# Optimization experiments

Hardware: AMD Instinct MI355X
Metric: run time of the kernel (lower is better)

## Reference

```python
import jax, jax.numpy as jnp
import numpy as np

NUM_MOVIES = 100000
MOVIE_FEAT = 128
USER_FEAT = 128
BATCH = 16384
N_NBRS = 50
D0, D1, D2 = 256, 256, 128  # layer_dims


def setup_inputs() -> dict:
    key = jax.random.key(0)
    ks = jax.random.split(key, 16)
    inp = {
        "users": jax.random.normal(ks[0], (BATCH, USER_FEAT), jnp.float32),
        "pos_movies": jax.random.normal(ks[1], (BATCH, MOVIE_FEAT), jnp.float32),
        "neg_movies": jax.random.normal(ks[2], (BATCH, MOVIE_FEAT), jnp.float32),
        "user_ids": jax.random.randint(ks[3], (BATCH,), 0, BATCH),
        "pos_movie_ids": jax.random.randint(ks[4], (BATCH,), 0, NUM_MOVIES),
        "neg_movie_ids": jax.random.randint(ks[5], (BATCH,), 0, NUM_MOVIES),
        "nbr_ids": jax.random.randint(ks[6], (BATCH, N_NBRS), 0, NUM_MOVIES),
        # learned params / buffers
        "movie_table": jax.random.normal(ks[7], (NUM_MOVIES, MOVIE_FEAT), jnp.float32),
        "Wu": jax.random.normal(ks[8], (USER_FEAT, D0), jnp.float32) * (1.0 / np.sqrt(USER_FEAT)),
        "bu": jnp.zeros((D0,), jnp.float32),
        "Wm": jax.random.normal(ks[9], (MOVIE_FEAT, D0), jnp.float32) * (1.0 / np.sqrt(MOVIE_FEAT)),
        "bm": jnp.zeros((D0,), jnp.float32),
        "W1": jax.random.normal(ks[10], (D0, D1), jnp.float32) * (1.0 / np.sqrt(D0)),
        "b1": jnp.zeros((D1,), jnp.float32),
        "W2": jax.random.normal(ks[11], (D1, D2), jnp.float32) * (1.0 / np.sqrt(D1)),
        "b2": jnp.zeros((D2,), jnp.float32),
    }
    return inp


def reference(users, pos_movies, neg_movies, user_ids, pos_movie_ids, neg_movie_ids,
              nbr_ids, movie_table, Wu, bu, Wm, bm, W1, b1, W2, b2):
    # user_projection / movie_projection
    user_emb = users @ Wu + bu                      # [B, D0]
    movie_emb = movie_table @ Wm + bm               # [N, D0]
    pos_emb = movie_emb[pos_movie_ids]              # [B, D0]
    neg_emb = movie_emb[neg_movie_ids]              # [B, D0]
    # vectorized replacement of the per-user neighbor gather + mean loop
    nbr_mean = jnp.mean(movie_emb[nbr_ids], axis=1)  # [B, N_NBRS, D0] -> [B, D0]
    user_emb = user_emb + nbr_mean
    x = jnp.stack([user_emb, pos_emb, neg_emb], axis=0)  # [3, B, D0]
    x = jax.nn.relu(x @ W1 + b1)
    x = jax.nn.relu(x @ W2 + b2)
    return (x[0], x[1], x[2])
```

## Files before the change

### kernel.cpp

```cpp
#include <hip/hip_runtime.h>
#include <hip/hip_bf16.h>

#define BATCH_N   16384
#define FEAT      128
#define NNBR      50
#define NUM_MOVIES_N 100000

typedef short  short8  __attribute__((ext_vector_type(8)));
typedef float  floatx4 __attribute__((ext_vector_type(4)));
typedef unsigned int u32;

__device__ __forceinline__ __hip_bfloat16 f2bf(float x) { return __float2bfloat16(x); }
__device__ __forceinline__ float bfb2f(short s) {
  union { u32 u; float f; } c; c.u = ((u32)(unsigned short)s) << 16; return c.f;
}

__device__ __forceinline__ void gld16(const __hip_bfloat16* g, __hip_bfloat16* l) {
  __builtin_amdgcn_global_load_lds(
      (const __attribute__((address_space(1))) u32*)g,
      (__attribute__((address_space(3))) u32*)l, 16, 0, 0);
}

__device__ __forceinline__ floatx4 mfma16(short8 a, short8 b, floatx4 c) {
  return __builtin_amdgcn_mfma_f32_16x16x32_bf16(a, b, c, 0, 0, 0);
}

#define WAITVM2 asm volatile("s_waitcnt vmcnt(2)" ::: "memory")
#define WAITVM0 asm volatile("s_waitcnt vmcnt(0)" ::: "memory")

#define CONV_BLOCKS (NUM_MOVIES_N * FEAT / (256 * 8))
__global__ __launch_bounds__(256) void prep_all(
    const float* __restrict__ t, __hip_bfloat16* __restrict__ tb,
    const float* __restrict__ Wu, const float* __restrict__ Wm,
    const float* __restrict__ W1, const float* __restrict__ W2,
    const float* __restrict__ bu, const float* __restrict__ bm,
    __hip_bfloat16* __restrict__ WcatT, __hip_bfloat16* __restrict__ WmT,
    __hip_bfloat16* __restrict__ W1T,  __hip_bfloat16* __restrict__ W2T,
    float* __restrict__ bc) {
  int bid = blockIdx.x;
  if (bid < CONV_BLOCKS) {
    size_t i = ((size_t)bid * 256 + threadIdx.x) * 8;
    float4 v0 = *(const float4*)(t + i);
    float4 v1 = *(const float4*)(t + i + 4);
    __hip_bfloat16 o[8];
    o[0] = f2bf(v0.x); o[1] = f2bf(v0.y); o[2] = f2bf(v0.z); o[3] = f2bf(v0.w);
    o[4] = f2bf(v1.x); o[5] = f2bf(v1.y); o[6] = f2bf(v1.z); o[7] = f2bf(v1.w);
    *(short8*)(tb + i) = *(short8*)o;
  } else {
    int idx = (bid - CONV_BLOCKS) * 256 + threadIdx.x;
    int n = idx & 255, k = idx >> 8;
    float v = (k < 128) ? Wu[k * 256 + n] : Wm[(k - 128) * 256 + n];
    WcatT[n * 256 + k] = f2bf(v);
    W1T[n * 256 + k]   = f2bf(W1[k * 256 + n]);
    if (k < 128) WmT[n * 128 + k] = f2bf(Wm[k * 256 + n]);
    if (idx < 32768) {
      int k2 = idx >> 7, n2 = idx & 127;
      W2T[n2 * 256 + k2] = f2bf(W2[k2 * 128 + n2]);
    }
    if (idx < 256) bc[idx] = bu[idx] + bm[idx];
  }
}

template <int K0, int NCOL, bool RELU, bool TOGLB>
__device__ __forceinline__ void layer(
    const __hip_bfloat16* Ain,
    const __hip_bfloat16* __restrict__ Wt, const float* __restrict__ bias,
    __hip_bfloat16* Olds, float* __restrict__ Oglb,
    int wid, int quad, int lrow) {
  constexpr int KK = K0 / 32;
  constexpr int JN = NCOL / 128;
  const int c0 = wid * JN * 16;

  short8 bfr[JN][KK];
  float  bv[JN];
  #pragma unroll
  for (int j = 0; j < JN; ++j) {
    #pragma unroll
    for (int kc = 0; kc < KK; ++kc)
      bfr[j][kc] = *(const short8*)(Wt + (size_t)(c0 + j * 16 + lrow) * K0 +
                                    kc * 32 + quad * 8);
    bv[j] = bias[c0 + j * 16 + lrow];
  }

  #pragma unroll
  for (int it = 0; it < 4; ++it) {
    int r = it * 16 + lrow;
    short8 af[KK];
    #pragma unroll
    for (int kc = 0; kc < KK; ++kc)
      af[kc] = *(const short8*)&Ain[r * K0 + (((kc * 4 + quad) ^ (r & 7)) << 3)];
    floatx4 pa[JN], pb[JN];
    #pragma unroll
    for (int j = 0; j < JN; ++j) { pa[j] = {}; pb[j] = {}; }
    #pragma unroll
    for (int kc = 0; kc < KK; kc += 2)
      #pragma unroll
      for (int j = 0; j < JN; ++j) {
        pa[j] = mfma16(af[kc],     bfr[j][kc],     pa[j]);
        pb[j] = mfma16(af[kc + 1], bfr[j][kc + 1], pb[j]);
      }
    #pragma unroll
    for (int j = 0; j < JN; ++j) {
      floatx4 a = pa[j] + pb[j];
      int col = c0 + j * 16 + lrow;
      #pragma unroll
      for (int rr = 0; rr < 4; ++rr) {
        int row = it * 16 + quad * 4 + rr;
        float v = a[rr] + bv[j];
        if (RELU) v = fmaxf(v, 0.f);
        if (TOGLB) {
          Oglb[(size_t)row * NCOL + col] = v;
        } else {
          int ch = col >> 3;
          Olds[row * 256 + (((ch ^ (row & 7)) << 3) | (col & 7))] = f2bf(v);
        }
      }
    }
  }
}

__global__ __launch_bounds__(512)
__attribute__((amdgpu_waves_per_eu(2, 2)))
void fused_mlp(
    const float* __restrict__ users,
    const __hip_bfloat16* __restrict__ tb,
    const int* __restrict__ pos_ids, const int* __restrict__ neg_ids,
    const int* __restrict__ nbr_ids,
    const __hip_bfloat16* __restrict__ WcatT,
    const __hip_bfloat16* __restrict__ WmT,
    const __hip_bfloat16* __restrict__ W1T,
    const __hip_bfloat16* __restrict__ W2T,
    const float* __restrict__ bc, const float* __restrict__ bmv,
    const float* __restrict__ b1, const float* __restrict__ b2,
    float* __restrict__ out) {
  __shared__ __hip_bfloat16 A_lds[64 * 256];
  __shared__ __hip_bfloat16 E_lds[64 * 256];

  const int t    = threadIdx.x;
  const int lane = t & 63, wid = t >> 6;
  const int quad = lane >> 4, lrow = lane & 15;

  int s, tile;
  if (blockIdx.x < 256) { s = 0; tile = blockIdx.x; }
  else { int k = blockIdx.x - 256; s = 1 + (k & 1); tile = k >> 1; }
  const long m0 = (long)tile * 64;

  if (s == 0) {
    const int rbase = wid << 3;
    const int* nbw = nbr_ids + (size_t)(m0 + rbase) * NNBR;
    int idreg[7];
    #pragma unroll
    for (int w = 0; w < 7; ++w) {
      int fl = w * 64 + lane;
      idreg[w] = nbw[fl < 8 * NNBR ? fl : 8 * NNBR - 1];
    }
    float2 uvr[8];
    #pragma unroll
    for (int r = 0; r < 8; ++r)
      uvr[r] = ((const float2*)(users + (size_t)(m0 + rbase + r) * FEAT))[lane];

    __hip_bfloat16* stg = E_lds + (wid << 11);

    auto getid = [&](int fb) -> int {
      int idx = fb + quad;
      int v = __shfl(idreg[fb >> 6], idx & 63, 64);
      if ((fb >> 6) != ((fb + 3) >> 6)) {
        int v2 = __shfl(idreg[(fb + 3) >> 6], idx & 63, 64);
        v = ((idx >> 6) == (fb >> 6)) ? v : v2;
      }
      return v;
    };
    auto issue = [&](int k) {
      int row = k / 7, c = k % 7;
      int id0 = getid(row * NNBR + c * 8);
      int id1 = getid(row * NNBR + c * 8 + 4);
      __hip_bfloat16* dst = stg + ((k & 1) << 10);
      gld16(tb + (size_t)id0 * FEAT + (lrow << 3), dst + (lane << 3));
      gld16(tb + (size_t)id1 * FEAT + (lrow << 3), dst + 512 + (lane << 3));
    };

    issue(0); issue(1);
    float acc[8] = {0.f, 0.f, 0.f, 0.f, 0.f, 0.f, 0.f, 0.f};
    #pragma unroll
    for (int k = 0; k < 56; ++k) {
      if (k < 55) { WAITVM2; } else { WAITVM0; }
      const __hip_bfloat16* b = stg + ((k & 1) << 10);
      int c = k % 7;
      short8 x0 = *(const short8*)(b + (lane << 3));
      if (c < 6) {
        short8 x1 = *(const short8*)(b + 512 + (lane << 3));
        #pragma unroll
        for (int e = 0; e < 8; ++e) { acc[e] += bfb2f(x0[e]); acc[e] += bfb2f(x1[e]); }
      } else if (quad < 2) {
        #pragma unroll
        for (int e = 0; e < 8; ++e) acc[e] += bfb2f(x0[e]);
      }
      if (c == 6) {
        int row = k / 7, r = rbase + row;
        __hip_bfloat16 o[8];
        #pragma unroll
        for (int e = 0; e < 8; ++e) {
          float v = acc[e];
          v += __shfl_xor(v, 16, 64);
          v += __shfl_xor(v, 32, 64);
          o[e] = f2bf(v * (1.f / NNBR));
          acc[e] = 0.f;
        }
        if (quad == 0) {
          int ch = 16 + lrow;
          *(short8*)(A_lds + r * 256 + ((ch ^ (r & 7)) << 3)) = *(short8*)o;
        }
        float2 uv = uvr[row];
        __hip_bfloat162 t0; t0.x = f2bf(uv.x); t0.y = f2bf(uv.y);
        int col = lane << 1, ch2 = col >> 3;
        *(__hip_bfloat162*)(A_lds + r * 256 + ((ch2 ^ (r & 7)) << 3) + (col & 7)) = t0;
      }
      __builtin_amdgcn_sched_barrier(0);
      if (k + 2 < 56) issue(k + 2);
    }
  } else {
    const int* ids = (s == 1) ? pos_ids : neg_ids;
    #pragma unroll
    for (int i = 0; i < 2; ++i) {
      int c = t + i * 512;
      int r = c >> 4, sl = c & 15;
      int id = ids[m0 + r];
      gld16(tb + ((size_t)id << 7) + ((sl ^ (r & 7)) << 3),
            A_lds + (c << 3));
    }
  }
  __syncthreads();

  if (s == 0)
    layer<256, 256, false, false>(A_lds, WcatT, bc, E_lds, nullptr,
                                  wid, quad, lrow);
  else
    layer<128, 256, false, false>(A_lds, WmT, bmv, E_lds, nullptr,
                                  wid, quad, lrow);
  __syncthreads();

  layer<256, 256, true, false>(E_lds, W1T, b1, A_lds, nullptr,
                               wid, quad, lrow);
  __syncthreads();

  layer<256, 128, true, true>(A_lds, W2T, b2, nullptr,
                              out + ((size_t)s * BATCH_N + m0) * 128,
                              wid, quad, lrow);
}

extern "C" void kernel_launch(void* const* d_in, const int* in_sizes, int n_in,
                              void* d_out, int out_size, void* d_ws, size_t ws_size,
                              hipStream_t stream) {
  const float* users   = (const float*)d_in[0];
  const int*   pos_ids = (const int*)d_in[4];
  const int*   neg_ids = (const int*)d_in[5];
  const int*   nbr_ids = (const int*)d_in[6];
  const float* table   = (const float*)d_in[7];
  const float* Wu = (const float*)d_in[8];
  const float* bu = (const float*)d_in[9];
  const float* Wm = (const float*)d_in[10];
  const float* bm = (const float*)d_in[11];
  const float* W1 = (const float*)d_in[12];
  const float* b1 = (const float*)d_in[13];
  const float* W2 = (const float*)d_in[14];
  const float* b2 = (const float*)d_in[15];
  float* out = (float*)d_out;

  char* p = (char*)d_ws;
  auto carve = [&](size_t bytes) { char* r = p; p += (bytes + 255) & ~(size_t)255; return r; };
  __hip_bfloat16* tb     = (__hip_bfloat16*)carve((size_t)NUM_MOVIES_N * FEAT * 2);
  __hip_bfloat16* WcatT  = (__hip_bfloat16*)carve(256 * 256 * 2);
  __hip_bfloat16* WmT    = (__hip_bfloat16*)carve(256 * 128 * 2);
  __hip_bfloat16* W1T    = (__hip_bfloat16*)carve(256 * 256 * 2);
  __hip_bfloat16* W2T    = (__hip_bfloat16*)carve(128 * 256 * 2);
  float*          bc     = (float*)carve(256 * 4);

  prep_all<<<CONV_BLOCKS + 256, 256, 0, stream>>>(
      table, tb, Wu, Wm, W1, W2, bu, bm, WcatT, WmT, W1T, W2T, bc);
  fused_mlp<<<3 * BATCH_N / 64, 512, 0, stream>>>(
      users, tb, pos_ids, neg_ids, nbr_ids, WcatT, WmT, W1T, W2T,
      bc, bm, b1, b2, out);
}
```

Measured before the change: 193.4 us.

## Halve user-tile rows and interleave user and movie blocks for load balance

User-path blocks, which do the expensive 50-neighbor gather, now handle 32 rows instead of 64, so their gather loop is half as long. User and pos/neg blocks are interleaved by block index so the heavy and light tiles are spread across the grid. The grid grows to 1024 blocks and the layer template gains a row-count parameter. The smaller user tiles load the weight fragments more times per row and use the MFMA units less efficiently in the MLP layers.

```diff
diff --git a/kernel.cpp b/kernel.cpp
--- a/kernel.cpp
+++ b/kernel.cpp
@@ -61,7 +61,7 @@
   }
 }
 
-template <int K0, int NCOL, bool RELU, bool TOGLB>
+template <int MROWS, int K0, int NCOL, bool RELU, bool TOGLB>
 __device__ __forceinline__ void layer(
     const __hip_bfloat16* Ain,
     const __hip_bfloat16* __restrict__ Wt, const float* __restrict__ bias,
@@ -83,7 +83,7 @@
   }
 
   #pragma unroll
-  for (int it = 0; it < 4; ++it) {
+  for (int it = 0; it < MROWS / 16; ++it) {
     int r = it * 16 + lrow;
     short8 af[KK];
     #pragma unroll
@@ -133,30 +133,31 @@
     const float* __restrict__ bc, const float* __restrict__ bmv,
     const float* __restrict__ b1, const float* __restrict__ b2,
     float* __restrict__ out) {
-  __shared__ __hip_bfloat16 A_lds[64 * 256];
-  __shared__ __hip_bfloat16 E_lds[64 * 256];
+  __shared__ char raw[65536];
+  __hip_bfloat16* A_lds = (__hip_bfloat16*)raw;
+  __hip_bfloat16* E_lds = (__hip_bfloat16*)(raw + 32768);
 
   const int t    = threadIdx.x;
   const int lane = t & 63, wid = t >> 6;
   const int quad = lane >> 4, lrow = lane & 15;
 
-  int s, tile;
-  if (blockIdx.x < 256) { s = 0; tile = blockIdx.x; }
-  else { int k = blockIdx.x - 256; s = 1 + (k & 1); tile = k >> 1; }
-  const long m0 = (long)tile * 64;
+  const int b = blockIdx.x;
+  int s; long m0;
+  if ((b & 1) == 0) { s = 0; m0 = (long)(b >> 1) * 32; }
+  else { int k = b >> 1; s = 1 + (k & 1); m0 = (long)(k >> 1) * 64; }
 
   if (s == 0) {
-    const int rbase = wid << 3;
+    const int rbase = wid << 2;
     const int* nbw = nbr_ids + (size_t)(m0 + rbase) * NNBR;
-    int idreg[7];
-    #pragma unroll
-    for (int w = 0; w < 7; ++w) {
+    int idreg[4];
+    #pragma unroll
+    for (int w = 0; w < 4; ++w) {
       int fl = w * 64 + lane;
-      idreg[w] = nbw[fl < 8 * NNBR ? fl : 8 * NNBR - 1];
-    }
-    float2 uvr[8];
-    #pragma unroll
-    for (int r = 0; r < 8; ++r)
+      idreg[w] = nbw[fl < 4 * NNBR ? fl : 4 * NNBR - 1];
+    }
+    float2 uvr[4];
+    #pragma unroll
+    for (int r = 0; r < 4; ++r)
       uvr[r] = ((const float2*)(users + (size_t)(m0 + rbase + r) * FEAT))[lane];
 
     __hip_bfloat16* stg = E_lds + (wid << 11);
@@ -182,13 +183,13 @@
     issue(0); issue(1);
     float acc[8] = {0.f, 0.f, 0.f, 0.f, 0.f, 0.f, 0.f, 0.f};
     #pragma unroll
-    for (int k = 0; k < 56; ++k) {
-      if (k < 55) { WAITVM2; } else { WAITVM0; }
-      const __hip_bfloat16* b = stg + ((k & 1) << 10);
+    for (int k = 0; k < 28; ++k) {
+      if (k < 27) { WAITVM2; } else { WAITVM0; }
+      const __hip_bfloat16* bb = stg + ((k & 1) << 10);
       int c = k % 7;
-      short8 x0 = *(const short8*)(b + (lane << 3));
+      short8 x0 = *(const short8*)(bb + (lane << 3));
       if (c < 6) {
-        short8 x1 = *(const short8*)(b + 512 + (lane << 3));
+        short8 x1 = *(const short8*)(bb + 512 + (lane << 3));
         #pragma unroll
         for (int e = 0; e < 8; ++e) { acc[e] += bfb2f(x0[e]); acc[e] += bfb2f(x1[e]); }
       } else if (quad < 2) {
@@ -216,7 +217,7 @@
         *(__hip_bfloat162*)(A_lds + r * 256 + ((ch2 ^ (r & 7)) << 3) + (col & 7)) = t0;
       }
       __builtin_amdgcn_sched_barrier(0);
-      if (k + 2 < 56) issue(k + 2);
+      if (k + 2 < 28) issue(k + 2);
     }
   } else {
     const int* ids = (s == 1) ? pos_ids : neg_ids;
@@ -231,21 +232,27 @@
   }
   __syncthreads();
 
-  if (s == 0)
-    layer<256, 256, false, false>(A_lds, WcatT, bc, E_lds, nullptr,
-                                  wid, quad, lrow);
-  else
-    layer<128, 256, false, false>(A_lds, WmT, bmv, E_lds, nullptr,
-                                  wid, quad, lrow);
-  __syncthreads();
-
-  layer<256, 256, true, false>(E_lds, W1T, b1, A_lds, nullptr,
-                               wid, quad, lrow);
-  __syncthreads();
-
-  layer<256, 128, true, true>(A_lds, W2T, b2, nullptr,
-                              out + ((size_t)s * BATCH_N + m0) * 128,
-                              wid, quad, lrow);
+  if (s == 0) {
+    layer<32, 256, 256, false, false>(A_lds, WcatT, bc, E_lds, nullptr,
+                                      wid, quad, lrow);
+    __syncthreads();
+    layer<32, 256, 256, true, false>(E_lds, W1T, b1, A_lds, nullptr,
+                                     wid, quad, lrow);
+    __syncthreads();
+    layer<32, 256, 128, true, true>(A_lds, W2T, b2, nullptr,
+                                    out + (size_t)m0 * 128,
+                                    wid, quad, lrow);
+  } else {
+    layer<64, 128, 256, false, false>(A_lds, WmT, bmv, E_lds, nullptr,
+                                      wid, quad, lrow);
+    __syncthreads();
+    layer<64, 256, 256, true, false>(E_lds, W1T, b1, A_lds, nullptr,
+                                     wid, quad, lrow);
+    __syncthreads();
+    layer<64, 256, 128, true, true>(A_lds, W2T, b2, nullptr,
+                                    out + ((size_t)s * BATCH_N + m0) * 128,
+                                    wid, quad, lrow);
+  }
 }
 
 extern "C" void kernel_launch(void* const* d_in, const int* in_sizes, int n_in,
@@ -277,7 +284,7 @@
 
   prep_all<<<CONV_BLOCKS + 256, 256, 0, stream>>>(
       table, tb, Wu, Wm, W1, W2, bu, bm, WcatT, WmT, W1T, W2T, bc);
-  fused_mlp<<<3 * BATCH_N / 64, 512, 0, stream>>>(
+  fused_mlp<<<1024, 512, 0, stream>>>(
       users, tb, pos_ids, neg_ids, nbr_ids, WcatT, WmT, W1T, W2T,
       bc, bm, b1, b2, out);
 }
```

Result: slower. 218.7 us (+13.1%).

## Split neighbor gather from user MLP blocks with global counter handoff

Applied to the files above, without the earlier changes.

Neighbor-mean blocks now only gather and average the neighbor embeddings, write them to a global bf16 scratch buffer, and signal through an atomic counter. A separate set of 256 user-MLP blocks spins until all gather blocks finish, then builds the concatenated input and runs the three layers. This decouples the latency-bound gather phase from the MFMA phase so the gather blocks can overlap with pos/neg MLP blocks. The cost is an extra global round trip for the neighbor means and a spin-wait that relies on the gather blocks being scheduled before the waiting blocks, which risks stalls or deadlock if the dispatch order changes.

```diff
diff --git a/kernel.cpp b/kernel.cpp
--- a/kernel.cpp
+++ b/kernel.cpp
@@ -36,7 +36,7 @@
     const float* __restrict__ bu, const float* __restrict__ bm,
     __hip_bfloat16* __restrict__ WcatT, __hip_bfloat16* __restrict__ WmT,
     __hip_bfloat16* __restrict__ W1T,  __hip_bfloat16* __restrict__ W2T,
-    float* __restrict__ bc) {
+    float* __restrict__ bc, unsigned int* __restrict__ ctr) {
   int bid = blockIdx.x;
   if (bid < CONV_BLOCKS) {
     size_t i = ((size_t)bid * 256 + threadIdx.x) * 8;
@@ -58,6 +58,7 @@
       W2T[n2 * 256 + k2] = f2bf(W2[k2 * 128 + n2]);
     }
     if (idx < 256) bc[idx] = bu[idx] + bm[idx];
+    if (idx == 0) *ctr = 0;
   }
 }
 
@@ -132,6 +133,7 @@
     const __hip_bfloat16* __restrict__ W2T,
     const float* __restrict__ bc, const float* __restrict__ bmv,
     const float* __restrict__ b1, const float* __restrict__ b2,
+    __hip_bfloat16* __restrict__ A_user, unsigned int* __restrict__ ctr,
     float* __restrict__ out) {
   __shared__ __hip_bfloat16 A_lds[64 * 256];
   __shared__ __hip_bfloat16 E_lds[64 * 256];
@@ -139,13 +141,10 @@
   const int t    = threadIdx.x;
   const int lane = t & 63, wid = t >> 6;
   const int quad = lane >> 4, lrow = lane & 15;
-
-  int s, tile;
-  if (blockIdx.x < 256) { s = 0; tile = blockIdx.x; }
-  else { int k = blockIdx.x - 256; s = 1 + (k & 1); tile = k >> 1; }
-  const long m0 = (long)tile * 64;
-
-  if (s == 0) {
+  const int b    = blockIdx.x;
+
+  if (b < 256) {
+    const long m0 = (long)b * 64;
     const int rbase = wid << 3;
     const int* nbw = nbr_ids + (size_t)(m0 + rbase) * NNBR;
     int idreg[7];
@@ -154,11 +153,6 @@
       int fl = w * 64 + lane;
       idreg[w] = nbw[fl < 8 * NNBR ? fl : 8 * NNBR - 1];
     }
-    float2 uvr[8];
-    #pragma unroll
-    for (int r = 0; r < 8; ++r)
-      uvr[r] = ((const float2*)(users + (size_t)(m0 + rbase + r) * FEAT))[lane];
-
     __hip_bfloat16* stg = E_lds + (wid << 11);
 
     auto getid = [&](int fb) -> int {
@@ -184,11 +178,11 @@
     #pragma unroll
     for (int k = 0; k < 56; ++k) {
       if (k < 55) { WAITVM2; } else { WAITVM0; }
-      const __hip_bfloat16* b = stg + ((k & 1) << 10);
+      const __hip_bfloat16* bb = stg + ((k & 1) << 10);
       int c = k % 7;
-      short8 x0 = *(const short8*)(b + (lane << 3));
+      short8 x0 = *(const short8*)(bb + (lane << 3));
       if (c < 6) {
-        short8 x1 = *(const short8*)(b + 512 + (lane << 3));
+        short8 x1 = *(const short8*)(bb + 512 + (lane << 3));
         #pragma unroll
         for (int e = 0; e < 8; ++e) { acc[e] += bfb2f(x0[e]); acc[e] += bfb2f(x1[e]); }
       } else if (quad < 2) {
@@ -196,7 +190,7 @@
         for (int e = 0; e < 8; ++e) acc[e] += bfb2f(x0[e]);
       }
       if (c == 6) {
-        int row = k / 7, r = rbase + row;
+        int row = k / 7;
         __hip_bfloat16 o[8];
         #pragma unroll
         for (int e = 0; e < 8; ++e) {
@@ -206,19 +200,24 @@
           o[e] = f2bf(v * (1.f / NNBR));
           acc[e] = 0.f;
         }
-        if (quad == 0) {
-          int ch = 16 + lrow;
-          *(short8*)(A_lds + r * 256 + ((ch ^ (r & 7)) << 3)) = *(short8*)o;
-        }
-        float2 uv = uvr[row];
-        __hip_bfloat162 t0; t0.x = f2bf(uv.x); t0.y = f2bf(uv.y);
-        int col = lane << 1, ch2 = col >> 3;
-        *(__hip_bfloat162*)(A_lds + r * 256 + ((ch2 ^ (r & 7)) << 3) + (col & 7)) = t0;
+        if (quad == 0)
+          *(short8*)(A_user + (size_t)(m0 + rbase + row) * 128 + (lrow << 3)) =
+              *(short8*)o;
       }
       __builtin_amdgcn_sched_barrier(0);
       if (k + 2 < 56) issue(k + 2);
     }
-  } else {
+    WAITVM0;
+    __syncthreads();
+    if (t == 0)
+      __hip_atomic_fetch_add(ctr, 1u, __ATOMIC_RELEASE, __HIP_MEMORY_SCOPE_AGENT);
+    return;
+  }
+
+  if (b < 768) {
+    int k = b - 256;
+    const int s = 1 + (k & 1);
+    const long m0 = (long)(k >> 1) * 64;
     const int* ids = (s == 1) ? pos_ids : neg_ids;
     #pragma unroll
     for (int i = 0; i < 2; ++i) {
@@ -228,24 +227,55 @@
       gld16(tb + ((size_t)id << 7) + ((sl ^ (r & 7)) << 3),
             A_lds + (c << 3));
     }
-  }
-  __syncthreads();
-
-  if (s == 0)
+    __syncthreads();
+
+    layer<128, 256, false, false>(A_lds, WmT, bmv, E_lds, nullptr,
+                                  wid, quad, lrow);
+    __syncthreads();
+    layer<256, 256, true, false>(E_lds, W1T, b1, A_lds, nullptr,
+                                 wid, quad, lrow);
+    __syncthreads();
+    layer<256, 128, true, true>(A_lds, W2T, b2, nullptr,
+                                out + ((size_t)s * BATCH_N + m0) * 128,
+                                wid, quad, lrow);
+    return;
+  }
+
+  {
+    const long m0 = (long)(b - 768) * 64;
+    if (t == 0) {
+      while (__hip_atomic_load(ctr, __ATOMIC_ACQUIRE, __HIP_MEMORY_SCOPE_AGENT)
+             < 256u)
+        __builtin_amdgcn_s_sleep(8);
+    }
+    __syncthreads();
+
+    const int rbase = wid << 3;
+    for (int rr = 0; rr < 8; ++rr) {
+      const int r = rbase | rr;
+      const size_t grow = (size_t)(m0 + r);
+      if (quad == 0) {
+        short8 m = *(const short8*)(A_user + grow * 128 + (lrow << 3));
+        int ch = 16 + lrow;
+        *(short8*)(A_lds + r * 256 + ((ch ^ (r & 7)) << 3)) = m;
+      }
+      float2 uv = ((const float2*)(users + grow * FEAT))[lane];
+      __hip_bfloat162 t0; t0.x = f2bf(uv.x); t0.y = f2bf(uv.y);
+      int col = lane << 1, ch2 = col >> 3;
+      *(__hip_bfloat162*)(A_lds + r * 256 + ((ch2 ^ (r & 7)) << 3) + (col & 7)) = t0;
+    }
+    __syncthreads();
+
     layer<256, 256, false, false>(A_lds, WcatT, bc, E_lds, nullptr,
                                   wid, quad, lrow);
-  else
-    layer<128, 256, false, false>(A_lds, WmT, bmv, E_lds, nullptr,
-                                  wid, quad, lrow);
-  __syncthreads();
-
-  layer<256, 256, true, false>(E_lds, W1T, b1, A_lds, nullptr,
-                               wid, quad, lrow);
-  __syncthreads();
-
-  layer<256, 128, true, true>(A_lds, W2T, b2, nullptr,
-                              out + ((size_t)s * BATCH_N + m0) * 128,
-                              wid, quad, lrow);
+    __syncthreads();
+    layer<256, 256, true, false>(E_lds, W1T, b1, A_lds, nullptr,
+                                 wid, quad, lrow);
+    __syncthreads();
+    layer<256, 128, true, true>(A_lds, W2T, b2, nullptr,
+                                out + (size_t)m0 * 128,
+                                wid, quad, lrow);
+  }
 }
 
 extern "C" void kernel_launch(void* const* d_in, const int* in_sizes, int n_in,
@@ -274,10 +304,12 @@
   __hip_bfloat16* W1T    = (__hip_bfloat16*)carve(256 * 256 * 2);
   __hip_bfloat16* W2T    = (__hip_bfloat16*)carve(128 * 256 * 2);
   float*          bc     = (float*)carve(256 * 4);
+  __hip_bfloat16* A_user = (__hip_bfloat16*)carve((size_t)BATCH_N * 128 * 2);
+  unsigned int*   ctr    = (unsigned int*)carve(256);
 
   prep_all<<<CONV_BLOCKS + 256, 256, 0, stream>>>(
-      table, tb, Wu, Wm, W1, W2, bu, bm, WcatT, WmT, W1T, W2T, bc);
-  fused_mlp<<<3 * BATCH_N / 64, 512, 0, stream>>>(
+      table, tb, Wu, Wm, W1, W2, bu, bm, WcatT, WmT, W1T, W2T, bc, ctr);
+  fused_mlp<<<1024, 512, 0, stream>>>(
       users, tb, pos_ids, neg_ids, nbr_ids, WcatT, WmT, W1T, W2T,
-      bc, bm, b1, b2, out);
-}
+      bc, bm, b1, b2, A_user, ctr, out);
+}
```

New measurement: 209.2 us. +8.1%, slower.
